# Optimization experiments

Measured on AMD Instinct MI355X. Metric: run time of the kernel, lower is better.

## Reference

```python
import jax, jax.numpy as jnp
import numpy as np

D_MODEL = 1024
N_HEADS = 16


def setup_inputs() -> dict:
    key = jax.random.key(0)
    ks = jax.random.split(key, 7)
    s = 0.02
    x = jax.random.normal(ks[0], (4, 2048, D_MODEL), dtype=jnp.float32)
    Wq = jax.random.normal(ks[1], (D_MODEL, D_MODEL), dtype=jnp.float32) * s
    Wk = jax.random.normal(ks[2], (D_MODEL, D_MODEL), dtype=jnp.float32) * s
    Wv = jax.random.normal(ks[3], (D_MODEL, D_MODEL), dtype=jnp.float32) * s
    bq = jax.random.normal(ks[4], (D_MODEL,), dtype=jnp.float32) * s
    bk = jax.random.normal(ks[5], (D_MODEL,), dtype=jnp.float32) * s
    bv = jax.random.normal(ks[6], (D_MODEL,), dtype=jnp.float32) * s
    return {"x": x, "Wq": Wq, "bq": bq, "Wk": Wk, "bk": bk, "Wv": Wv, "bv": bv}


def reference(x, Wq, bq, Wk, bk, Wv, bv):
    B, S, D = x.shape
    H = N_HEADS
    hd = D // H
    # torch Linear: y = x @ W.T + b
    q = (x @ Wq.T + bq).reshape(B, S, H, hd).transpose(0, 2, 1, 3)  # [B,H,S,hd]
    k = (x @ Wk.T + bk).reshape(B, S, H, hd).transpose(0, 2, 1, 3)
    v = (x @ Wv.T + bv).reshape(B, S, H, hd).transpose(0, 2, 1, 3)
    # NOTE: source scales by sqrt(d_model), not sqrt(head_dim)
    scores = jnp.einsum('bhqd,bhkd->bhqk', q, k) / jnp.sqrt(jnp.float32(D))
    attn = jax.nn.softmax(scores, axis=-1)
    out = jnp.einsum('bhqk,bhkd->bhqd', attn, v)  # [B,H,S,hd]
    return out.transpose(0, 2, 1, 3).reshape(B, S, D)
```

## Files before the change

kernel.cpp:

```cpp
#include <hip/hip_runtime.h>
#include <hip/hip_bf16.h>

#define D_MODEL 1024
#define NHEADS  16
#define HD      64
#define BATCH   4
#define SEQ     2048

#define XELEMS (BATCH * SEQ * D_MODEL)
#define WELEMS (D_MODEL * D_MODEL)

typedef __attribute__((ext_vector_type(8))) short v8s;
typedef __attribute__((ext_vector_type(4))) float v4f;

using bf16 = __hip_bfloat16;

#define GLD_LDS(gp, lp) \
    __builtin_amdgcn_global_load_lds((const __attribute__((address_space(1))) void*)(gp), \
                                     (__attribute__((address_space(3))) void*)(lp), 16, 0, 0)

#if __has_builtin(__builtin_amdgcn_exp2f)
#define EXP2(x) __builtin_amdgcn_exp2f(x)
#else
#define EXP2(x) exp2f(x)
#endif

__device__ __forceinline__ unsigned int f2bf(float f) {
    union { float f; unsigned int u; } c; c.f = f;
    unsigned int u = c.u;
    u += 0x7fffu + ((u >> 16) & 1u);
    return u >> 16;
}

__device__ __forceinline__ unsigned int pack_bf16_hu(float lo, float hi) {
    unsigned int a = __float_as_uint(lo) + 0x8000u;
    unsigned int b = __float_as_uint(hi) + 0x8000u;
    return __builtin_amdgcn_perm(b, a, 0x07060302u);
}

__device__ __forceinline__ uint4 cvt8(const float* p) {
    float4 f0 = ((const float4*)p)[0];
    float4 f1 = ((const float4*)p)[1];
    uint4 r;
    r.x = f2bf(f0.x) | (f2bf(f0.y) << 16);
    r.y = f2bf(f0.z) | (f2bf(f0.w) << 16);
    r.z = f2bf(f1.x) | (f2bf(f1.y) << 16);
    r.w = f2bf(f1.z) | (f2bf(f1.w) << 16);
    return r;
}

__device__ __forceinline__ void qswap32(unsigned int &a, unsigned int &b) {
#if __has_builtin(__builtin_amdgcn_permlane32_swap)
    auto r = __builtin_amdgcn_permlane32_swap(a, b, false, false);
    a = (unsigned int)r[0]; b = (unsigned int)r[1];
#else
    unsigned int ax = (unsigned int)__shfl_xor((int)a, 32, 64);
    unsigned int bx = (unsigned int)__shfl_xor((int)b, 32, 64);
    if (threadIdx.x & 32) { a = bx; } else { b = ax; }
#endif
}
__device__ __forceinline__ void qswap16(unsigned int &a, unsigned int &b) {
#if __has_builtin(__builtin_amdgcn_permlane16_swap)
    auto r = __builtin_amdgcn_permlane16_swap(a, b, false, false);
    a = (unsigned int)r[0]; b = (unsigned int)r[1];
#else
    unsigned int ax = (unsigned int)__shfl_xor((int)a, 16, 64);
    unsigned int bx = (unsigned int)__shfl_xor((int)b, 16, 64);
    if (threadIdx.x & 16) { a = bx; } else { b = ax; }
#endif
}

__global__ void detect_dtype(const unsigned short* __restrict__ x16,
                             int* __restrict__ flag) {
    int lane = threadIdx.x;
    unsigned short v = x16[2 * lane];
    int e = (v >> 7) & 0xff;
    bool plaus = (e >= 90) && (e <= 141);
    unsigned long long m = __ballot(plaus);
    if (lane == 0) *flag = (__popcll(m) >= 48) ? 1 : 0;
}

__global__ __launch_bounds__(256) void convert_inputs(
    const void* __restrict__ x,
    const void* __restrict__ wq, const void* __restrict__ wk,
    const void* __restrict__ wv,
    const void* __restrict__ bq, const void* __restrict__ bk,
    const void* __restrict__ bv,
    bf16* __restrict__ xbf, bf16* __restrict__ wbf, bf16* __restrict__ bbf,
    const int* __restrict__ flag)
{
    const int isbf = *flag;
    long g = (long)blockIdx.x * 256 + threadIdx.x;
    const long xg = XELEMS / 8;
    const long wg = WELEMS / 8;
    const long bg = D_MODEL / 8;
    const void* src; bf16* dst; long off;
    if      (g < xg)                  { src = x;  dst = xbf;              off = g; }
    else if (g < xg + wg)             { src = wq; dst = wbf;              off = g - xg; }
    else if (g < xg + 2*wg)           { src = wk; dst = wbf + WELEMS;     off = g - xg - wg; }
    else if (g < xg + 3*wg)           { src = wv; dst = wbf + 2*WELEMS;   off = g - xg - 2*wg; }
    else if (g < xg + 3*wg + bg)      { src = bq; dst = bbf;              off = g - xg - 3*wg; }
    else if (g < xg + 3*wg + 2*bg)    { src = bk; dst = bbf + D_MODEL;    off = g - xg - 3*wg - bg; }
    else if (g < xg + 3*wg + 3*bg)    { src = bv; dst = bbf + 2*D_MODEL;  off = g - xg - 3*wg - 2*bg; }
    else return;
    uint4 r = isbf ? ((const uint4*)src)[off]
                   : cvt8((const float*)src + off * 8);
    ((uint4*)dst)[off] = r;
}

__global__ __launch_bounds__(256, 3) void qkv_gemm(
    const bf16* __restrict__ xbf, const bf16* __restrict__ wbf,
    const bf16* __restrict__ bbf,
    bf16* __restrict__ qout, bf16* __restrict__ kout, bf16* __restrict__ vout)
{
    __shared__ bf16 Atile[16 * 512];
    __shared__ bf16 Btile[16 * 512];

    const int z = blockIdx.z;
    const bf16* W    = wbf + (size_t)z * WELEMS;
    const bf16* bias = bbf + z * D_MODEL;
    bf16* out = (z == 0) ? qout : (z == 1) ? kout : vout;
    const float scale = (z == 0) ? (1.4426950408889634f / 32.0f) : 1.0f;

    const int tid  = threadIdx.x;
    const int lane = tid & 63;
    const int wave = tid >> 6;
    const int m0w  = (wave >> 1) * 64;
    const int n0w  = (wave & 1) * 64;
    const int m_base = blockIdx.x * 128;
    const int n_base = blockIdx.y * 128;

    const int lm   = lane & 15;
    const int quad = lane >> 4;

    const int slm = lane >> 2;
    const int sq  = lane & 3;
    const int fidx = (lm * 4 + quad) * 8;

    v4f acc[4][4] = {};

    for (int k0 = 0; k0 < D_MODEL; k0 += 64) {
        __syncthreads();
        #pragma unroll
        for (int j = 0; j < 4; ++j) {
            int c  = wave * 4 + j;
            int rt = c >> 1, kb = c & 1;
            const bf16* ga = xbf + (size_t)(m_base + rt * 16 + slm) * D_MODEL
                                 + k0 + kb * 32 + sq * 8;
            const bf16* gb = W   + (size_t)(n_base + rt * 16 + slm) * D_MODEL
                                 + k0 + kb * 32 + sq * 8;
            GLD_LDS(ga, Atile + c * 512);
            GLD_LDS(gb, Btile + c * 512);
        }
        __syncthreads();

        #pragma unroll
        for (int kb = 0; kb < 2; ++kb) {
            v8s af[4], bf[4];
            #pragma unroll
            for (int mt = 0; mt < 4; ++mt)
                af[mt] = *(const v8s*)(Atile + (((m0w >> 4) + mt) * 2 + kb) * 512 + fidx);
            #pragma unroll
            for (int nt = 0; nt < 4; ++nt)
                bf[nt] = *(const v8s*)(Btile + (((n0w >> 4) + nt) * 2 + kb) * 512 + fidx);
            #pragma unroll
            for (int mt = 0; mt < 4; ++mt)
                #pragma unroll
                for (int nt = 0; nt < 4; ++nt)
                    acc[mt][nt] = __builtin_amdgcn_mfma_f32_16x16x32_bf16(
                        af[mt], bf[nt], acc[mt][nt], 0, 0, 0);
        }
    }

    #pragma unroll
    for (int nt = 0; nt < 4; ++nt) {
        int n = n_base + n0w + nt * 16 + lm;
        float bb = __bfloat162float(bias[n]);
        int h = n >> 6, d = n & 63;
        #pragma unroll
        for (int mt = 0; mt < 4; ++mt) {
            if (z == 2) {
                int m = m_base + m0w + mt * 16 + quad * 4;
                int b = m >> 11, s = m & (SEQ - 1);
                float p0 = acc[mt][nt][0] + bb;
                float p1 = acc[mt][nt][1] + bb;
                float p2 = acc[mt][nt][2] + bb;
                float p3 = acc[mt][nt][3] + bb;
                uint2 pk;
                pk.x = pack_bf16_hu(p0, p1);
                pk.y = pack_bf16_hu(p2, p3);
                size_t bh = (size_t)(b * NHEADS + h);
                *(uint2*)(out + (((bh << 6) + d) << 11) + s) = pk;
            } else {
                #pragma unroll
                for (int r = 0; r < 4; ++r) {
                    int m = m_base + m0w + mt * 16 + quad * 4 + r;
                    int b = m >> 11, s = m & (SEQ - 1);
                    float vv = (acc[mt][nt][r] + bb) * scale;
                    size_t bh = (size_t)(b * NHEADS + h);
                    out[(((bh << 11) + s) << 6) + d] = __float2bfloat16(vv);
                }
            }
        }
    }
}

__global__ __launch_bounds__(256, 4) void attn(
    const bf16* __restrict__ q, const bf16* __restrict__ k,
    const bf16* __restrict__ vT, void* __restrict__ out,
    const int* __restrict__ flag)
{
    __shared__ bf16 Ks[2][8 * 512];
    __shared__ bf16 Vt[2][8 * 512];

    const int isbf = *flag;

    const int l   = blockIdx.x;
    const int idx = l >> 3;
    const int q0  = (idx & 15) * 128;
    const int bh  = (l & 7) + ((idx >> 4) << 3);
    const int b   = bh >> 4, h = bh & 15;
    const size_t head_base  = (size_t)bh * SEQ * HD;
    const size_t head_baseT = (size_t)bh * HD * SEQ;

    const int tid  = threadIdx.x;
    const int lane = tid & 63;
    const int wave = tid >> 6;
    const int lm   = lane & 15;
    const int quad = lane >> 4;

    const int slm = lane >> 2;
    const int sq  = lane & 3;
    const int fidx = (lm * 4 + quad) * 8;

    v8s aq[2][2];
    #pragma unroll
    for (int mt = 0; mt < 2; ++mt)
        #pragma unroll
        for (int kb = 0; kb < 2; ++kb)
            aq[mt][kb] = *(const v8s*)(q + head_base
                          + (size_t)(q0 + wave * 32 + mt * 16 + lm) * HD
                          + kb * 32 + quad * 8);

    float l_acc[2] = { 0.0f, 0.0f };
    v4f   O[2][4] = {};

    typedef union { v8s v; unsigned int u[4]; } AB;

    auto stage = [&](int bi, int kv0_) {
        #pragma unroll
        for (int j = 0; j < 2; ++j) {
            int c  = wave * 2 + j;
            int kt = c >> 1, kb = c & 1;
            const bf16* ga = k + head_base
                + (size_t)(kv0_ + kt * 16 + slm) * HD + kb * 32 + sq * 8;
            GLD_LDS(ga, &Ks[bi][c * 512]);
        }
        #pragma unroll
        for (int j = 0; j < 2; ++j) {
            int c  = wave * 2 + j;
            int g1 = c >> 2, dt = c & 3;
            const bf16* gv = vT + head_baseT
                + (size_t)(dt * 16 + slm) * SEQ + kv0_ + sq * 16 + g1 * 8;
            GLD_LDS(gv, &Vt[bi][c * 512]);
        }
    };

    stage(0, 0);
    __syncthreads();

    const int NT = SEQ / 64;
    for (int t = 0; t < NT; ++t) {
        const int cur = t & 1;
        if (t + 1 < NT) stage(cur ^ 1, (t + 1) * 64);

        v4f sc[4][2] = {};
        #pragma unroll
        for (int kb = 0; kb < 2; ++kb) {
            v8s kf[4];
            #pragma unroll
            for (int kt = 0; kt < 4; ++kt)
                kf[kt] = *(const v8s*)(&Ks[cur][(kt * 2 + kb) * 512] + fidx);
            #pragma unroll
            for (int kt = 0; kt < 4; ++kt)
                #pragma unroll
                for (int mt = 0; mt < 2; ++mt)
                    sc[kt][mt] = __builtin_amdgcn_mfma_f32_16x16x32_bf16(
                        kf[kt], aq[mt][kb], sc[kt][mt], 0, 0, 0);
        }

        unsigned int pw[2][4][2];
        #pragma unroll
        for (int mt = 0; mt < 2; ++mt) {
            #pragma unroll
            for (int kt = 0; kt < 4; ++kt) {
                float p0 = EXP2(sc[kt][mt][0]);
                float p1 = EXP2(sc[kt][mt][1]);
                float p2 = EXP2(sc[kt][mt][2]);
                float p3 = EXP2(sc[kt][mt][3]);
                l_acc[mt] += (p0 + p1) + (p2 + p3);
                pw[mt][kt][0] = pack_bf16_hu(p0, p1);
                pw[mt][kt][1] = pack_bf16_hu(p2, p3);
            }
        }

        #pragma unroll
        for (int mt = 0; mt < 2; ++mt)
            #pragma unroll
            for (int kt0 = 0; kt0 < 2; ++kt0)
                #pragma unroll
                for (int j = 0; j < 2; ++j)
                    qswap32(pw[mt][kt0][j], pw[mt][kt0 + 2][j]);
        #pragma unroll
        for (int mt = 0; mt < 2; ++mt)
            #pragma unroll
            for (int g1 = 0; g1 < 2; ++g1)
                #pragma unroll
                for (int j = 0; j < 2; ++j)
                    qswap16(pw[mt][2 * g1][j], pw[mt][2 * g1 + 1][j]);

        #pragma unroll
        for (int kk = 0; kk < 2; ++kk) {
            v8s bv8[4];
            #pragma unroll
            for (int dt = 0; dt < 4; ++dt)
                bv8[dt] = *(const v8s*)(&Vt[cur][(kk * 4 + dt) * 512] + fidx);
            #pragma unroll
            for (int mt = 0; mt < 2; ++mt) {
                AB a;
                a.u[0] = pw[mt][2 * kk + 0][0];
                a.u[1] = pw[mt][2 * kk + 0][1];
                a.u[2] = pw[mt][2 * kk + 1][0];
                a.u[3] = pw[mt][2 * kk + 1][1];
                #pragma unroll
                for (int dt = 0; dt < 4; ++dt)
                    O[mt][dt] = __builtin_amdgcn_mfma_f32_16x16x32_bf16(
                        a.v, bv8[dt], O[mt][dt], 0, 0, 0);
            }
        }

        __syncthreads();
    }

    float inv[2];
    #pragma unroll
    for (int mt = 0; mt < 2; ++mt) {
        float lsum = l_acc[mt];
        lsum += __shfl_xor(lsum, 16, 64);
        lsum += __shfl_xor(lsum, 32, 64);
        inv[mt] = 1.0f / lsum;
    }

    #pragma unroll
    for (int mt = 0; mt < 2; ++mt) {
        #pragma unroll
        for (int r = 0; r < 4; ++r) {
            float ir = __shfl(inv[mt], quad * 4 + r, 64);
            int s = q0 + wave * 32 + mt * 16 + quad * 4 + r;
            #pragma unroll
            for (int dt = 0; dt < 4; ++dt) {
                int d = dt * 16 + lm;
                size_t off = (size_t)(b * SEQ + s) * D_MODEL + h * HD + d;
                float val = O[mt][dt][r] * ir;
                if (isbf) ((bf16*)out)[off] = __float2bfloat16(val);
                else      ((float*)out)[off] = val;
            }
        }
    }
}

extern "C" void kernel_launch(void* const* d_in, const int* in_sizes, int n_in,
                              void* d_out, int out_size, void* d_ws, size_t ws_size,
                              hipStream_t stream) {
    const void* x  = d_in[0];
    const void* Wq = d_in[1];
    const void* bq = d_in[2];
    const void* Wk = d_in[3];
    const void* bk = d_in[4];
    const void* Wv = d_in[5];
    const void* bv = d_in[6];

    char* ws = (char*)d_ws;
    int*  flag = (int*)ws;
    bf16* wbf  = (bf16*)(ws + 256);
    bf16* bbf  = (bf16*)(ws + 256 + 3 * (size_t)WELEMS * 2);
    bf16* qws  = (bf16*)(ws + 256 + 3 * (size_t)WELEMS * 2 + 8192);
    const size_t per = (size_t)BATCH * NHEADS * SEQ * HD;
    bf16* kws = qws + per;
    bf16* vws = kws + per;

    bf16* xbf = (bf16*)d_out;

    detect_dtype<<<1, 64, 0, stream>>>((const unsigned short*)x, flag);

    const long ngroups = (long)XELEMS / 8 + 3L * (WELEMS / 8) + 3L * (D_MODEL / 8);
    convert_inputs<<<(int)((ngroups + 255) / 256), 256, 0, stream>>>(
        x, Wq, Wk, Wv, bq, bk, bv, xbf, wbf, bbf, flag);

    dim3 g1(64, 8, 3);
    qkv_gemm<<<g1, 256, 0, stream>>>(xbf, wbf, bbf, qws, kws, vws);

    attn<<<1024, 256, 0, stream>>>(qws, kws, vws, d_out, flag);
}
```

Baseline: 234.5 us.

## Double-buffer QKV GEMM LDS tiles, inline dtype detection, use hardware bf16 pack

```diff
diff --git a/kernel.cpp b/kernel.cpp
--- a/kernel.cpp
+++ b/kernel.cpp
@@ -36,6 +36,12 @@
     unsigned int a = __float_as_uint(lo) + 0x8000u;
     unsigned int b = __float_as_uint(hi) + 0x8000u;
     return __builtin_amdgcn_perm(b, a, 0x07060302u);
+}
+
+__device__ __forceinline__ unsigned int cvtpk_bf16(float lo, float hi) {
+    unsigned int r;
+    asm("v_cvt_pk_bf16_f32 %0, %1, %2" : "=v"(r) : "v"(lo), "v"(hi));
+    return r;
 }
 
 __device__ __forceinline__ uint4 cvt8(const float* p) {
@@ -49,6 +55,14 @@
     return r;
 }
 
+__device__ __forceinline__ int detect_isbf(const unsigned short* x16, int tid) {
+    unsigned short v = x16[2 * (tid & 63)];
+    int e = (v >> 7) & 0xff;
+    bool plaus = (e >= 90) && (e <= 141);
+    unsigned long long m = __ballot(plaus);
+    return (__popcll(m) >= 48) ? 1 : 0;
+}
+
 __device__ __forceinline__ void qswap32(unsigned int &a, unsigned int &b) {
 #if __has_builtin(__builtin_amdgcn_permlane32_swap)
     auto r = __builtin_amdgcn_permlane32_swap(a, b, false, false);
@@ -70,26 +84,15 @@
 #endif
 }
 
-__global__ void detect_dtype(const unsigned short* __restrict__ x16,
-                             int* __restrict__ flag) {
-    int lane = threadIdx.x;
-    unsigned short v = x16[2 * lane];
-    int e = (v >> 7) & 0xff;
-    bool plaus = (e >= 90) && (e <= 141);
-    unsigned long long m = __ballot(plaus);
-    if (lane == 0) *flag = (__popcll(m) >= 48) ? 1 : 0;
-}
-
 __global__ __launch_bounds__(256) void convert_inputs(
     const void* __restrict__ x,
     const void* __restrict__ wq, const void* __restrict__ wk,
     const void* __restrict__ wv,
     const void* __restrict__ bq, const void* __restrict__ bk,
     const void* __restrict__ bv,
-    bf16* __restrict__ xbf, bf16* __restrict__ wbf, bf16* __restrict__ bbf,
-    const int* __restrict__ flag)
+    bf16* __restrict__ xbf, bf16* __restrict__ wbf, bf16* __restrict__ bbf)
 {
-    const int isbf = *flag;
+    const int isbf = detect_isbf((const unsigned short*)x, threadIdx.x);
     long g = (long)blockIdx.x * 256 + threadIdx.x;
     const long xg = XELEMS / 8;
     const long wg = WELEMS / 8;
@@ -113,8 +116,8 @@
     const bf16* __restrict__ bbf,
     bf16* __restrict__ qout, bf16* __restrict__ kout, bf16* __restrict__ vout)
 {
-    __shared__ bf16 Atile[16 * 512];
-    __shared__ bf16 Btile[16 * 512];
+    __shared__ bf16 Atile[2][8 * 512];
+    __shared__ bf16 Btile[2][8 * 512];
 
     const int z = blockIdx.z;
     const bf16* W    = wbf + (size_t)z * WELEMS;
@@ -139,37 +142,42 @@
 
     v4f acc[4][4] = {};
 
-    for (int k0 = 0; k0 < D_MODEL; k0 += 64) {
+    auto stage = [&](int bi, int k0_) {
+        #pragma unroll
+        for (int j = 0; j < 2; ++j) {
+            int rt = wave * 2 + j;
+            const bf16* ga = xbf + (size_t)(m_base + rt * 16 + slm) * D_MODEL
+                                 + k0_ + sq * 8;
+            const bf16* gb = W   + (size_t)(n_base + rt * 16 + slm) * D_MODEL
+                                 + k0_ + sq * 8;
+            GLD_LDS(ga, &Atile[bi][rt * 512]);
+            GLD_LDS(gb, &Btile[bi][rt * 512]);
+        }
+    };
+
+    stage(0, 0);
+    __syncthreads();
+
+    const int NKT = D_MODEL / 32;
+    for (int t = 0; t < NKT; ++t) {
+        const int cur = t & 1;
+        if (t + 1 < NKT) stage(cur ^ 1, (t + 1) * 32);
+
+        v8s af[4], bf[4];
+        #pragma unroll
+        for (int mt = 0; mt < 4; ++mt)
+            af[mt] = *(const v8s*)(&Atile[cur][((m0w >> 4) + mt) * 512] + fidx);
+        #pragma unroll
+        for (int nt = 0; nt < 4; ++nt)
+            bf[nt] = *(const v8s*)(&Btile[cur][((n0w >> 4) + nt) * 512] + fidx);
+        #pragma unroll
+        for (int mt = 0; mt < 4; ++mt)
+            #pragma unroll
+            for (int nt = 0; nt < 4; ++nt)
+                acc[mt][nt] = __builtin_amdgcn_mfma_f32_16x16x32_bf16(
+                    af[mt], bf[nt], acc[mt][nt], 0, 0, 0);
+
         __syncthreads();
-        #pragma unroll
-        for (int j = 0; j < 4; ++j) {
-            int c  = wave * 4 + j;
-            int rt = c >> 1, kb = c & 1;
-            const bf16* ga = xbf + (size_t)(m_base + rt * 16 + slm) * D_MODEL
-                                 + k0 + kb * 32 + sq * 8;
-            const bf16* gb = W   + (size_t)(n_base + rt * 16 + slm) * D_MODEL
-                                 + k0 + kb * 32 + sq * 8;
-            GLD_LDS(ga, Atile + c * 512);
-            GLD_LDS(gb, Btile + c * 512);
-        }
-        __syncthreads();
-
-        #pragma unroll
-        for (int kb = 0; kb < 2; ++kb) {
-            v8s af[4], bf[4];
-            #pragma unroll
-            for (int mt = 0; mt < 4; ++mt)
-                af[mt] = *(const v8s*)(Atile + (((m0w >> 4) + mt) * 2 + kb) * 512 + fidx);
-            #pragma unroll
-            for (int nt = 0; nt < 4; ++nt)
-                bf[nt] = *(const v8s*)(Btile + (((n0w >> 4) + nt) * 2 + kb) * 512 + fidx);
-            #pragma unroll
-            for (int mt = 0; mt < 4; ++mt)
-                #pragma unroll
-                for (int nt = 0; nt < 4; ++nt)
-                    acc[mt][nt] = __builtin_amdgcn_mfma_f32_16x16x32_bf16(
-                        af[mt], bf[nt], acc[mt][nt], 0, 0, 0);
-        }
     }
 
     #pragma unroll
@@ -208,12 +216,12 @@
 __global__ __launch_bounds__(256, 4) void attn(
     const bf16* __restrict__ q, const bf16* __restrict__ k,
     const bf16* __restrict__ vT, void* __restrict__ out,
-    const int* __restrict__ flag)
+    const unsigned short* __restrict__ x16)
 {
     __shared__ bf16 Ks[2][8 * 512];
     __shared__ bf16 Vt[2][8 * 512];
 
-    const int isbf = *flag;
+    const int isbf = detect_isbf(x16, threadIdx.x);
 
     const int l   = blockIdx.x;
     const int idx = l >> 3;
@@ -299,8 +307,8 @@
                 float p2 = EXP2(sc[kt][mt][2]);
                 float p3 = EXP2(sc[kt][mt][3]);
                 l_acc[mt] += (p0 + p1) + (p2 + p3);
-                pw[mt][kt][0] = pack_bf16_hu(p0, p1);
-                pw[mt][kt][1] = pack_bf16_hu(p2, p3);
+                pw[mt][kt][0] = cvtpk_bf16(p0, p1);
+                pw[mt][kt][1] = cvtpk_bf16(p2, p3);
             }
         }
 
@@ -381,7 +389,6 @@
     const void* bv = d_in[6];
 
     char* ws = (char*)d_ws;
-    int*  flag = (int*)ws;
     bf16* wbf  = (bf16*)(ws + 256);
     bf16* bbf  = (bf16*)(ws + 256 + 3 * (size_t)WELEMS * 2);
     bf16* qws  = (bf16*)(ws + 256 + 3 * (size_t)WELEMS * 2 + 8192);
@@ -391,14 +398,13 @@
 
     bf16* xbf = (bf16*)d_out;
 
-    detect_dtype<<<1, 64, 0, stream>>>((const unsigned short*)x, flag);
-
     const long ngroups = (long)XELEMS / 8 + 3L * (WELEMS / 8) + 3L * (D_MODEL / 8);
     convert_inputs<<<(int)((ngroups + 255) / 256), 256, 0, stream>>>(
-        x, Wq, Wk, Wv, bq, bk, bv, xbf, wbf, bbf, flag);
+        x, Wq, Wk, Wv, bq, bk, bv, xbf, wbf, bbf);
 
     dim3 g1(64, 8, 3);
     qkv_gemm<<<g1, 256, 0, stream>>>(xbf, wbf, bbf, qws, kws, vws);
 
-    attn<<<1024, 256, 0, stream>>>(qws, kws, vws, d_out, flag);
-}
+    attn<<<1024, 256, 0, stream>>>(qws, kws, vws, d_out,
+                                   (const unsigned short*)x);
+}
```

After: 240.0 us. 1.02x slower.
